# Kernel tuning notes

Hardware: AMD Instinct MI355X
Metric: run time of the kernel (lower is better)

## Reference

```python
import jax, jax.numpy as jnp
import numpy as np

NUM_HEADS = 8
NUM_POINTS = 9


def _bilinear_sample(img, gx, gy):
    """grid_sample, mode=bilinear, padding=zeros, align_corners=True.
    img: (B, C, H, W); gx, gy: (B, M) pixel coords. Returns (B, C, M)."""
    Bc, C, H, W = img.shape
    imgf = img.reshape(Bc, C, H * W)
    x0 = jnp.floor(gx)
    y0 = jnp.floor(gy)
    wx1 = gx - x0
    wy1 = gy - y0

    def corner(xi, yi, w):
        valid = (xi >= 0) & (xi < W) & (yi >= 0) & (yi < H)
        xi_c = jnp.clip(xi, 0, W - 1).astype(jnp.int32)
        yi_c = jnp.clip(yi, 0, H - 1).astype(jnp.int32)
        idx = yi_c * W + xi_c  # (B, M)
        g = jax.vmap(lambda im, ix: im[:, ix])(imgf, idx)  # (B, C, M)
        return g * (w * valid)[:, None, :]

    return (corner(x0, y0, (1 - wx1) * (1 - wy1))
            + corner(x0 + 1, y0, wx1 * (1 - wy1))
            + corner(x0, y0 + 1, (1 - wx1) * wy1)
            + corner(x0 + 1, y0 + 1, wx1 * wy1))


def setup_inputs() -> dict:
    key = jax.random.key(0)
    ks = jax.random.split(key, 6)
    B, Hp, Wp, T, D = 4, 64, 64, 3, 256
    N = Hp * Wp
    Hh, P = NUM_HEADS, NUM_POINTS
    x = jax.random.normal(ks[0], (B, N, T, D), dtype=jnp.float32)
    # offset/attn projections: small random (orig inits them to 0, which is degenerate for testing)
    W_off = jax.random.normal(ks[1], (D, Hh * P * 2), dtype=jnp.float32) * 0.01
    b_off = jnp.zeros((Hh * P * 2,), dtype=jnp.float32)
    W_attn = jax.random.normal(ks[2], (D, Hh * P), dtype=jnp.float32) * 0.01
    b_attn = jnp.zeros((Hh * P,), dtype=jnp.float32)
    W_v = jax.random.normal(ks[3], (D, D), dtype=jnp.float32) * 0.02
    b_v = jnp.zeros((D,), dtype=jnp.float32)
    W_o = jax.random.normal(ks[4], (D, D), dtype=jnp.float32) * 0.02
    b_o = jnp.zeros((D,), dtype=jnp.float32)
    return {"x": x, "W_off": W_off, "b_off": b_off, "W_attn": W_attn,
            "b_attn": b_attn, "W_v": W_v, "b_v": b_v, "W_o": W_o,
            "b_o": b_o, "Hp": Hp, "Wp": Wp}


def reference(x, W_off, b_off, W_attn, b_attn, W_v, b_v, W_o, b_o, Hp, Wp):
    B, N, T, D = x.shape
    Hh, P = NUM_HEADS, NUM_POINTS
    dh = D // Hh

    query = x[:, :, T // 2]  # (B, N, D) middle frame
    offset = (query @ W_off + b_off).reshape(B, N, Hh, P, 2)
    attn = jax.nn.softmax((query @ W_attn + b_attn).reshape(B, N, Hh, P), axis=-1)

    # reference points in [-1, 1], xy order (x = width coord)
    gh, gw = jnp.meshgrid(jnp.arange(Hp, dtype=jnp.float32),
                          jnp.arange(Wp, dtype=jnp.float32), indexing='ij')
    ref = jnp.stack([gw, gh], axis=-1).reshape(N, 2)
    ref = ref / jnp.asarray([Wp - 1, Hp - 1], dtype=jnp.float32) * 2 - 1

    loc = ref[None, :, None, None, :] + offset  # (B, N, H, P, 2) normalized

    value = (x @ W_v + b_v).reshape(B, N, T, Hh, dh)
    # (B, H, T, dh, N) -> (B*H*T, dh, Hp, Wp)
    val = jnp.transpose(value, (0, 3, 2, 4, 1)).reshape(B * Hh * T, dh, Hp, Wp)

    # per-(b,h) grid, shared across frames; fold T into batch of the sampler
    grid = jnp.transpose(loc, (0, 2, 1, 3, 4))  # (B, H, N, P, 2)
    grid = jnp.broadcast_to(grid[:, :, None], (B, Hh, T, N, P, 2))
    grid = grid.reshape(B * Hh * T, N * P, 2)
    gx = (grid[..., 0] + 1) * 0.5 * (Wp - 1)
    gy = (grid[..., 1] + 1) * 0.5 * (Hp - 1)

    sampled = _bilinear_sample(val, gx, gy)  # (B*H*T, dh, N*P)
    sampled = sampled.reshape(B, Hh, T, dh, N, P)

    # weighted sum over points, summed over frames
    out = jnp.einsum('bhtdnp,bnhp->bnhd', sampled, attn).reshape(B, N, D)
    return out @ W_o + b_o
```

## Files before the change

kernel.cpp:

```cpp
#include <hip/hip_runtime.h>
#include <hip/hip_bf16.h>
#include <hip/hip_fp16.h>


#define NH_ 8
#define DH_ 32
#define MM_ 16384

typedef __attribute__((ext_vector_type(8))) short bf16x8;
typedef __attribute__((ext_vector_type(4))) short bf16x4;
typedef __attribute__((ext_vector_type(4))) float f32x4;

static __device__ __forceinline__ unsigned short f2bf(float f) {
  unsigned int u = __float_as_uint(f);
  u = (u + 0x7fff + ((u >> 16) & 1)) >> 16;
  return (unsigned short)u;
}
static __device__ __forceinline__ float bf2f(unsigned short h) {
  return __uint_as_float(((unsigned int)h) << 16);
}

__global__ __launch_bounds__(256) void prep(
    const float* __restrict__ x,
    const float* __restrict__ W_off, const float* __restrict__ W_attn,
    const float* __restrict__ W_v, const float* __restrict__ W_o,
    const float* __restrict__ b_off, const float* __restrict__ b_attn,
    unsigned short* __restrict__ ash, unsigned short* __restrict__ asl,
    unsigned short* __restrict__ xmh, unsigned short* __restrict__ xml,
    unsigned short* __restrict__ wvh, unsigned short* __restrict__ wvl,
    unsigned short* __restrict__ wch, unsigned short* __restrict__ wcl,
    unsigned short* __restrict__ woh, unsigned short* __restrict__ wol,
    float* __restrict__ bcat) {
  const int bid = blockIdx.x, t = threadIdx.x;
  if (bid < 4096) {
    const int gid = bid * 256 + t;
    const int row = gid >> 6, c4 = (gid & 63) * 4;
    const float* xr = x + (size_t)row * 768 + c4;
    float4 a0 = *(const float4*)xr;
    float4 a1 = *(const float4*)(xr + 256);
    float4 a2 = *(const float4*)(xr + 512);
    float s[4] = {a0.x + a1.x + a2.x, a0.y + a1.y + a2.y,
                  a0.z + a1.z + a2.z, a0.w + a1.w + a2.w};
    float m[4] = {a1.x, a1.y, a1.z, a1.w};
    bf16x4 shv, slv, mhv, mlv;
#pragma unroll
    for (int j = 0; j < 4; ++j) {
      unsigned short h = f2bf(s[j]);
      shv[j] = (short)h; slv[j] = (short)f2bf(s[j] - bf2f(h));
      unsigned short h2 = f2bf(m[j]);
      mhv[j] = (short)h2; mlv[j] = (short)f2bf(m[j] - bf2f(h2));
    }
    const size_t o = (size_t)row * 256 + c4;
    *(bf16x4*)(ash + o) = shv;  *(bf16x4*)(asl + o) = slv;
    *(bf16x4*)(xmh + o) = mhv;  *(bf16x4*)(xml + o) = mlv;
  } else {
    const int n = bid - 4096;
    {
      float v = W_v[(size_t)t * 256 + n];
      unsigned short h = f2bf(v);
      wvh[n * 256 + t] = h; wvl[n * 256 + t] = f2bf(v - bf2f(h));
    }
    {
      float v = W_o[(size_t)t * 256 + n];
      unsigned short h = f2bf(v);
      woh[n * 256 + t] = h; wol[n * 256 + t] = f2bf(v - bf2f(h));
    }
    if (n < 216) {
      float v = (n < 144) ? W_off[(size_t)t * 144 + n] : W_attn[(size_t)t * 72 + (n - 144)];
      unsigned short h = f2bf(v);
      wch[n * 256 + t] = h; wcl[n * 256 + t] = f2bf(v - bf2f(h));
    }
    if (n == 0 && t < 216) bcat[t] = (t < 144) ? b_off[t] : b_attn[t - 144];
  }
}

__global__ __launch_bounds__(256, 4) void mgemm01(
    const unsigned short* __restrict__ Ahi, const unsigned short* __restrict__ Alo,
    const unsigned short* __restrict__ Xmh, const unsigned short* __restrict__ Xml,
    const unsigned short* __restrict__ Wvh, const unsigned short* __restrict__ Wvl,
    const unsigned short* __restrict__ Wch, const unsigned short* __restrict__ Wcl,
    const float* __restrict__ b_v, const float* __restrict__ bcat,
    __half* __restrict__ valsum, float* __restrict__ proj) {
  __shared__ unsigned short Ah[64][64], Al[64][64], Bh[64][64], Bl[64][64];
  const int mode1 = blockIdx.y >= 4;
  const int n0 = (blockIdx.y & 3) * 64;
  const int m0 = blockIdx.x * 64;
  const int tid = threadIdx.x, wid = tid >> 6, lane = tid & 63;
  const int am = (wid >> 1) * 32, bn = (wid & 1) * 32;
  const int fr = lane & 15, kg = lane >> 4;
  const unsigned short* Ahs = mode1 ? Xmh : Ahi;
  const unsigned short* Als = mode1 ? Xml : Alo;
  const unsigned short* Bhs = mode1 ? Wch : Wvh;
  const unsigned short* Bls = mode1 ? Wcl : Wvl;

  const int r0s = tid >> 3, c0s = tid & 7;
  const int r1s = r0s + 32;
  const int d0s = r0s * 64 + ((c0s ^ (r0s & 7)) * 8);
  const int d1s = r1s * 64 + ((c0s ^ (r1s & 7)) * 8);

  f32x4 acc[2][2];
#pragma unroll
  for (int i = 0; i < 2; ++i)
#pragma unroll
    for (int j = 0; j < 2; ++j) acc[i][j] = (f32x4)(0.f);

  bf16x8 pah[2], pal[2], pbh[2], pbl[2];

#define LOADT01(k0)                                                          \
  {                                                                          \
    size_t a0 = (size_t)(m0 + r0s) * 256 + (k0) + c0s * 8;                   \
    size_t a1 = (size_t)(m0 + r1s) * 256 + (k0) + c0s * 8;                   \
    pah[0] = *(const bf16x8*)(Ahs + a0); pal[0] = *(const bf16x8*)(Als + a0);\
    pah[1] = *(const bf16x8*)(Ahs + a1); pal[1] = *(const bf16x8*)(Als + a1);\
    int nr0 = n0 + r0s, nr1 = n0 + r1s;                                      \
    size_t b0 = (size_t)nr0 * 256 + (k0) + c0s * 8;                          \
    size_t b1 = (size_t)nr1 * 256 + (k0) + c0s * 8;                          \
    if (!mode1 || nr0 < 216) {                                               \
      pbh[0] = *(const bf16x8*)(Bhs + b0); pbl[0] = *(const bf16x8*)(Bls + b0);\
    } else { pbh[0] = (bf16x8)(short)0; pbl[0] = (bf16x8)(short)0; }         \
    if (!mode1 || nr1 < 216) {                                               \
      pbh[1] = *(const bf16x8*)(Bhs + b1); pbl[1] = *(const bf16x8*)(Bls + b1);\
    } else { pbh[1] = (bf16x8)(short)0; pbl[1] = (bf16x8)(short)0; }         \
  }

#define WRITET()                                                             \
  {                                                                          \
    *(bf16x8*)(&Ah[0][0] + d0s) = pah[0]; *(bf16x8*)(&Al[0][0] + d0s) = pal[0];\
    *(bf16x8*)(&Ah[0][0] + d1s) = pah[1]; *(bf16x8*)(&Al[0][0] + d1s) = pal[1];\
    *(bf16x8*)(&Bh[0][0] + d0s) = pbh[0]; *(bf16x8*)(&Bl[0][0] + d0s) = pbl[0];\
    *(bf16x8*)(&Bh[0][0] + d1s) = pbh[1]; *(bf16x8*)(&Bl[0][0] + d1s) = pbl[1];\
  }

#define COMPUTET()                                                           \
  _Pragma("unroll")                                                          \
  for (int ks = 0; ks < 2; ++ks) {                                           \
    const int kc = ks * 4 + kg;                                              \
    bf16x8 ah[2], al[2], bh[2], bl[2];                                       \
    _Pragma("unroll")                                                        \
    for (int mi = 0; mi < 2; ++mi) {                                         \
      int m = am + mi * 16 + fr;                                             \
      int o = m * 64 + ((kc ^ (m & 7)) * 8);                                 \
      ah[mi] = *(const bf16x8*)(&Ah[0][0] + o);                              \
      al[mi] = *(const bf16x8*)(&Al[0][0] + o);                              \
    }                                                                        \
    _Pragma("unroll")                                                        \
    for (int ni = 0; ni < 2; ++ni) {                                         \
      int nn = bn + ni * 16 + fr;                                            \
      int o = nn * 64 + ((kc ^ (nn & 7)) * 8);                               \
      bh[ni] = *(const bf16x8*)(&Bh[0][0] + o);                              \
      bl[ni] = *(const bf16x8*)(&Bl[0][0] + o);                              \
    }                                                                        \
    _Pragma("unroll")                                                        \
    for (int mi = 0; mi < 2; ++mi)                                           \
      _Pragma("unroll")                                                      \
      for (int ni = 0; ni < 2; ++ni) {                                       \
        acc[mi][ni] = __builtin_amdgcn_mfma_f32_16x16x32_bf16(ah[mi], bh[ni], acc[mi][ni], 0, 0, 0);\
        acc[mi][ni] = __builtin_amdgcn_mfma_f32_16x16x32_bf16(ah[mi], bl[ni], acc[mi][ni], 0, 0, 0);\
        acc[mi][ni] = __builtin_amdgcn_mfma_f32_16x16x32_bf16(al[mi], bh[ni], acc[mi][ni], 0, 0, 0);\
      }                                                                      \
  }

  LOADT01(0);
  WRITET();
  __syncthreads();
#pragma unroll
  for (int t = 0; t < 4; ++t) {
    if (t < 3) LOADT01((t + 1) * 64);
    COMPUTET();
    __syncthreads();
    if (t < 3) { WRITET(); __syncthreads(); }
  }

  const int ro = kg * 4;
#pragma unroll
  for (int mi = 0; mi < 2; ++mi)
#pragma unroll
    for (int ni = 0; ni < 2; ++ni) {
      int col = n0 + bn + ni * 16 + fr;
      if (mode1 && col >= 216) continue;
      int rowb = m0 + am + mi * 16 + ro;
      float bv = mode1 ? bcat[col] : b_v[col] * 3.f;
#pragma unroll
      for (int r = 0; r < 4; ++r) {
        int grow = rowb + r;
        float v = acc[mi][ni][r] + bv;
        if (mode1) {
          proj[(size_t)grow * 216 + col] = v;
        } else {
          int b = grow >> 12, nn2 = grow & 4095;
          int h = col >> 5, d = col & 31;
          valsum[(((size_t)(b * NH_ + h) << 12) + nn2) * DH_ + d] = __float2half_rn(v);
        }
      }
    }
#undef LOADT01
#undef WRITET
#undef COMPUTET
}

__global__ __launch_bounds__(256, 4) void mgemm2(
    const unsigned short* __restrict__ Ahi, const unsigned short* __restrict__ Alo,
    const unsigned short* __restrict__ Bhs, const unsigned short* __restrict__ Bls,
    const float* __restrict__ bias, float* __restrict__ Cout) {
  __shared__ unsigned short Ah[64][64], Al[64][64], Bh[64][64], Bl[64][64];
  const int n0 = blockIdx.y * 64;
  const int m0 = blockIdx.x * 64;
  const int tid = threadIdx.x, wid = tid >> 6, lane = tid & 63;
  const int am = (wid >> 1) * 32, bn = (wid & 1) * 32;
  const int fr = lane & 15, kg = lane >> 4;

  const int r0s = tid >> 3, c0s = tid & 7;
  const int r1s = r0s + 32;
  const int d0s = r0s * 64 + ((c0s ^ (r0s & 7)) * 8);
  const int d1s = r1s * 64 + ((c0s ^ (r1s & 7)) * 8);

  f32x4 acc[2][2];
#pragma unroll
  for (int i = 0; i < 2; ++i)
#pragma unroll
    for (int j = 0; j < 2; ++j) acc[i][j] = (f32x4)(0.f);

  bf16x8 pah[2], pal[2], pbh[2], pbl[2];

#define LOADT2(k0)                                                           \
  {                                                                          \
    size_t a0 = (size_t)(m0 + r0s) * 256 + (k0) + c0s * 8;                   \
    size_t a1 = (size_t)(m0 + r1s) * 256 + (k0) + c0s * 8;                   \
    pah[0] = *(const bf16x8*)(Ahi + a0); pal[0] = *(const bf16x8*)(Alo + a0);\
    pah[1] = *(const bf16x8*)(Ahi + a1); pal[1] = *(const bf16x8*)(Alo + a1);\
    size_t b0 = (size_t)(n0 + r0s) * 256 + (k0) + c0s * 8;                   \
    size_t b1 = (size_t)(n0 + r1s) * 256 + (k0) + c0s * 8;                   \
    pbh[0] = *(const bf16x8*)(Bhs + b0); pbl[0] = *(const bf16x8*)(Bls + b0);\
    pbh[1] = *(const bf16x8*)(Bhs + b1); pbl[1] = *(const bf16x8*)(Bls + b1);\
  }

#define WRITET2()                                                            \
  {                                                                          \
    *(bf16x8*)(&Ah[0][0] + d0s) = pah[0]; *(bf16x8*)(&Al[0][0] + d0s) = pal[0];\
    *(bf16x8*)(&Ah[0][0] + d1s) = pah[1]; *(bf16x8*)(&Al[0][0] + d1s) = pal[1];\
    *(bf16x8*)(&Bh[0][0] + d0s) = pbh[0]; *(bf16x8*)(&Bl[0][0] + d0s) = pbl[0];\
    *(bf16x8*)(&Bh[0][0] + d1s) = pbh[1]; *(bf16x8*)(&Bl[0][0] + d1s) = pbl[1];\
  }

#define COMPUTET2()                                                          \
  _Pragma("unroll")                                                          \
  for (int ks = 0; ks < 2; ++ks) {                                           \
    const int kc = ks * 4 + kg;                                              \
    bf16x8 ah[2], al[2], bh[2], bl[2];                                       \
    _Pragma("unroll")                                                        \
    for (int mi = 0; mi < 2; ++mi) {                                         \
      int m = am + mi * 16 + fr;                                             \
      int o = m * 64 + ((kc ^ (m & 7)) * 8);                                 \
      ah[mi] = *(const bf16x8*)(&Ah[0][0] + o);                              \
      al[mi] = *(const bf16x8*)(&Al[0][0] + o);                              \
    }                                                                        \
    _Pragma("unroll")                                                        \
    for (int ni = 0; ni < 2; ++ni) {                                         \
      int nn = bn + ni * 16 + fr;                                            \
      int o = nn * 64 + ((kc ^ (nn & 7)) * 8);                               \
      bh[ni] = *(const bf16x8*)(&Bh[0][0] + o);                              \
      bl[ni] = *(const bf16x8*)(&Bl[0][0] + o);                              \
    }                                                                        \
    _Pragma("unroll")                                                        \
    for (int mi = 0; mi < 2; ++mi)                                           \
      _Pragma("unroll")                                                      \
      for (int ni = 0; ni < 2; ++ni) {                                       \
        acc[mi][ni] = __builtin_amdgcn_mfma_f32_16x16x32_bf16(ah[mi], bh[ni], acc[mi][ni], 0, 0, 0);\
        acc[mi][ni] = __builtin_amdgcn_mfma_f32_16x16x32_bf16(ah[mi], bl[ni], acc[mi][ni], 0, 0, 0);\
        acc[mi][ni] = __builtin_amdgcn_mfma_f32_16x16x32_bf16(al[mi], bh[ni], acc[mi][ni], 0, 0, 0);\
      }                                                                      \
  }

  LOADT2(0);
  WRITET2();
  __syncthreads();
#pragma unroll
  for (int t = 0; t < 4; ++t) {
    if (t < 3) LOADT2((t + 1) * 64);
    COMPUTET2();
    __syncthreads();
    if (t < 3) { WRITET2(); __syncthreads(); }
  }

  const int ro = kg * 4;
#pragma unroll
  for (int mi = 0; mi < 2; ++mi)
#pragma unroll
    for (int ni = 0; ni < 2; ++ni) {
      int col = n0 + bn + ni * 16 + fr;
      int rowb = m0 + am + mi * 16 + ro;
      float bv = bias[col];
#pragma unroll
      for (int r = 0; r < 4; ++r)
        Cout[(size_t)(rowb + r) * 256 + col] = acc[mi][ni][r] + bv;
    }
#undef LOADT2
#undef WRITET2
#undef COMPUTET2
}

struct IW { int idx; float w; };

__global__ __launch_bounds__(256) void sample4(const __half* __restrict__ valsum,
                                               const float* __restrict__ proj,
                                               unsigned short* __restrict__ ihi,
                                               unsigned short* __restrict__ ilo) {
  const int bid = blockIdx.x;
  const int wv = threadIdx.x >> 6;
  const int lane = threadIdx.x & 63;
  const int row = ((bid & 7) << 11) + ((bid >> 3) << 2) + wv;
  const int b = row >> 12, n = row & 4095;

  __shared__ IW cwi[4][72][4];
  __shared__ float sap[4][76];

  const float* pr = proj + (size_t)row * 216;
  if (lane < 8) {
    const float* pa = pr + 144 + lane * 9;
    float lg[9], mx = -1e30f;
#pragma unroll
    for (int p = 0; p < 9; ++p) { lg[p] = pa[p]; mx = fmaxf(mx, lg[p]); }
    float s = 0.f;
#pragma unroll
    for (int p = 0; p < 9; ++p) { lg[p] = __expf(lg[p] - mx); s += lg[p]; }
    float inv = 1.f / s;
#pragma unroll
    for (int p = 0; p < 9; ++p) sap[wv][lane * 9 + p] = lg[p] * inv;
  }
  __syncthreads();
  for (int e = lane; e < 72; e += 64) {
    float ox = pr[e * 2], oy = pr[e * 2 + 1];
    float gx = (float)(n & 63) + ox * 31.5f;
    float gy = (float)(n >> 6) + oy * 31.5f;
    float fx0 = floorf(gx), fy0 = floorf(gy);
    float wx1 = gx - fx0, wy1 = gy - fy0;
    float wx0 = 1.f - wx1, wy0 = 1.f - wy1;
    int x0 = (int)fx0, y0 = (int)fy0, x1 = x0 + 1, y1 = y0 + 1;
    bool vx0 = (x0 >= 0) & (x0 < 64), vx1 = (x1 >= 0) & (x1 < 64);
    bool vy0 = (y0 >= 0) & (y0 < 64), vy1 = (y1 >= 0) & (y1 < 64);
    int x0c = min(max(x0, 0), 63), x1c = min(max(x1, 0), 63);
    int y0c = min(max(y0, 0), 63), y1c = min(max(y1, 0), 63);
    const float a = sap[wv][e];
    cwi[wv][e][0] = IW{(y0c * 64 + x0c) * DH_, (vx0 & vy0) ? wx0 * wy0 * a : 0.f};
    cwi[wv][e][1] = IW{(y0c * 64 + x1c) * DH_, (vx1 & vy0) ? wx1 * wy0 * a : 0.f};
    cwi[wv][e][2] = IW{(y1c * 64 + x0c) * DH_, (vx0 & vy1) ? wx0 * wy1 * a : 0.f};
    cwi[wv][e][3] = IW{(y1c * 64 + x1c) * DH_, (vx1 & vy1) ? wx1 * wy1 * a : 0.f};
  }
  __syncthreads();

  const int h = lane >> 3, d4 = (lane & 7) * 4;
  const __half* vb = valsum + (((size_t)(b * NH_ + h)) << 12) * DH_ + d4;
  float ax = 0.f, ay = 0.f, az = 0.f, aw = 0.f;
#pragma unroll
  for (int pb = 0; pb < 9; pb += 3) {
    float2 v[24]; float w[12];
#pragma unroll
    for (int q = 0; q < 3; ++q) {
      const int hp = h * 9 + pb + q;
#pragma unroll
      for (int c = 0; c < 4; ++c) {
        IW e = cwi[wv][hp][c];
        const __half2* p = (const __half2*)(vb + e.idx);
        v[(q * 4 + c) * 2 + 0] = __half22float2(p[0]);
        v[(q * 4 + c) * 2 + 1] = __half22float2(p[1]);
        w[q * 4 + c] = e.w;
      }
    }
#pragma unroll
    for (int j = 0; j < 12; ++j) {
      ax += w[j] * v[j * 2].x;     ay += w[j] * v[j * 2].y;
      az += w[j] * v[j * 2 + 1].x; aw += w[j] * v[j * 2 + 1].y;
    }
  }
  float av[4] = {ax, ay, az, aw};
  bf16x4 hv, lv;
#pragma unroll
  for (int j = 0; j < 4; ++j) {
    unsigned short hh = f2bf(av[j]);
    hv[j] = (short)hh;
    lv[j] = (short)f2bf(av[j] - bf2f(hh));
  }
  const size_t o = (size_t)row * 256 + lane * 4;
  *(bf16x4*)(ihi + o) = hv;
  *(bf16x4*)(ilo + o) = lv;
}

extern "C" void kernel_launch(void* const* d_in, const int* in_sizes, int n_in,
                              void* d_out, int out_size, void* d_ws, size_t ws_size,
                              hipStream_t stream) {
  const float* x      = (const float*)d_in[0];
  const float* W_off  = (const float*)d_in[1];
  const float* b_off  = (const float*)d_in[2];
  const float* W_attn = (const float*)d_in[3];
  const float* b_attn = (const float*)d_in[4];
  const float* W_v    = (const float*)d_in[5];
  const float* b_v    = (const float*)d_in[6];
  const float* W_o    = (const float*)d_in[7];
  const float* b_o    = (const float*)d_in[8];
  float* out = (float*)d_out;

  __half* valsum = (__half*)d_ws;
  float* proj    = (float*)(valsum + (size_t)MM_ * 256);
  float* bcat    = proj + (size_t)MM_ * 216;
  unsigned short* ash = (unsigned short*)(bcat + 256);
  unsigned short* asl = ash + (size_t)MM_ * 256;
  unsigned short* xmh = asl + (size_t)MM_ * 256;
  unsigned short* xml = xmh + (size_t)MM_ * 256;
  unsigned short* wvh = xml + (size_t)MM_ * 256;
  unsigned short* wvl = wvh + 65536;
  unsigned short* wch = wvl + 65536;
  unsigned short* wcl = wch + 55296;
  unsigned short* woh = wcl + 55296;
  unsigned short* wol = woh + 65536;
  unsigned short* ihi = ash;
  unsigned short* ilo = asl;

  prep<<<dim3(4352), dim3(256), 0, stream>>>(x, W_off, W_attn, W_v, W_o, b_off, b_attn,
                                             ash, asl, xmh, xml,
                                             wvh, wvl, wch, wcl, woh, wol, bcat);
  mgemm01<<<dim3(256, 8), dim3(256), 0, stream>>>(ash, asl, xmh, xml, wvh, wvl, wch, wcl,
                                                  b_v, bcat, valsum, proj);
  sample4<<<dim3(4096), dim3(256), 0, stream>>>(valsum, proj, ihi, ilo);
  mgemm2<<<dim3(256, 4), dim3(256), 0, stream>>>(ihi, ilo, woh, wol, b_o, out);
}
```

Baseline: 162.2 us.

## Switch split-bf16 GEMMs to fp16 and drop low-part weights for value/output

Replaces the bf16 hi/lo split with an fp16 hi/lo split, which has more mantissa bits. This lets the W_v and W_o weights be stored as a single fp16 without a low part, cutting each MFMA group for those GEMMs from three to two products and removing the Bl loads and shared stores. Only the offset/attention projection keeps a three-term product, and both GEMM grids are flattened to 1D with a remapped block order. The sampler now loads fp16x4 vectors directly. fp16 has less range than bf16, and dropping the weight low parts reduces accuracy.

```diff
diff --git a/kernel.cpp b/kernel.cpp
--- a/kernel.cpp
+++ b/kernel.cpp
@@ -1,23 +1,21 @@
 #include <hip/hip_runtime.h>
 #include <hip/hip_bf16.h>
-#include <hip/hip_fp16.h>
 
 
 #define NH_ 8
 #define DH_ 32
 #define MM_ 16384
 
-typedef __attribute__((ext_vector_type(8))) short bf16x8;
-typedef __attribute__((ext_vector_type(4))) short bf16x4;
+typedef __attribute__((ext_vector_type(8))) _Float16 f16x8;
+typedef __attribute__((ext_vector_type(4))) _Float16 f16x4;
 typedef __attribute__((ext_vector_type(4))) float f32x4;
 
-static __device__ __forceinline__ unsigned short f2bf(float f) {
-  unsigned int u = __float_as_uint(f);
-  u = (u + 0x7fff + ((u >> 16) & 1)) >> 16;
-  return (unsigned short)u;
-}
-static __device__ __forceinline__ float bf2f(unsigned short h) {
-  return __uint_as_float(((unsigned int)h) << 16);
+struct HL { _Float16 h, l; };
+static __device__ __forceinline__ HL fsplit(float f) {
+  HL r;
+  r.h = (_Float16)f;
+  r.l = (_Float16)(f - (float)r.h);
+  return r;
 }
 
 __global__ __launch_bounds__(256) void prep(
@@ -25,11 +23,10 @@
     const float* __restrict__ W_off, const float* __restrict__ W_attn,
     const float* __restrict__ W_v, const float* __restrict__ W_o,
     const float* __restrict__ b_off, const float* __restrict__ b_attn,
-    unsigned short* __restrict__ ash, unsigned short* __restrict__ asl,
-    unsigned short* __restrict__ xmh, unsigned short* __restrict__ xml,
-    unsigned short* __restrict__ wvh, unsigned short* __restrict__ wvl,
-    unsigned short* __restrict__ wch, unsigned short* __restrict__ wcl,
-    unsigned short* __restrict__ woh, unsigned short* __restrict__ wol,
+    _Float16* __restrict__ ash, _Float16* __restrict__ asl,
+    _Float16* __restrict__ xmh, _Float16* __restrict__ xml,
+    _Float16* __restrict__ wv, _Float16* __restrict__ wch,
+    _Float16* __restrict__ wcl, _Float16* __restrict__ wo,
     float* __restrict__ bcat) {
   const int bid = blockIdx.x, t = threadIdx.x;
   if (bid < 4096) {
@@ -42,56 +39,50 @@
     float s[4] = {a0.x + a1.x + a2.x, a0.y + a1.y + a2.y,
                   a0.z + a1.z + a2.z, a0.w + a1.w + a2.w};
     float m[4] = {a1.x, a1.y, a1.z, a1.w};
-    bf16x4 shv, slv, mhv, mlv;
+    f16x4 shv, slv, mhv, mlv;
 #pragma unroll
     for (int j = 0; j < 4; ++j) {
-      unsigned short h = f2bf(s[j]);
-      shv[j] = (short)h; slv[j] = (short)f2bf(s[j] - bf2f(h));
-      unsigned short h2 = f2bf(m[j]);
-      mhv[j] = (short)h2; mlv[j] = (short)f2bf(m[j] - bf2f(h2));
+      HL sj = fsplit(s[j]);
+      shv[j] = sj.h; slv[j] = sj.l;
+      HL mj = fsplit(m[j]);
+      mhv[j] = mj.h; mlv[j] = mj.l;
     }
     const size_t o = (size_t)row * 256 + c4;
-    *(bf16x4*)(ash + o) = shv;  *(bf16x4*)(asl + o) = slv;
-    *(bf16x4*)(xmh + o) = mhv;  *(bf16x4*)(xml + o) = mlv;
+    *(f16x4*)(ash + o) = shv;  *(f16x4*)(asl + o) = slv;
+    *(f16x4*)(xmh + o) = mhv;  *(f16x4*)(xml + o) = mlv;
   } else {
     const int n = bid - 4096;
-    {
-      float v = W_v[(size_t)t * 256 + n];
-      unsigned short h = f2bf(v);
-      wvh[n * 256 + t] = h; wvl[n * 256 + t] = f2bf(v - bf2f(h));
-    }
-    {
-      float v = W_o[(size_t)t * 256 + n];
-      unsigned short h = f2bf(v);
-      woh[n * 256 + t] = h; wol[n * 256 + t] = f2bf(v - bf2f(h));
-    }
+    wv[n * 256 + t] = (_Float16)W_v[(size_t)t * 256 + n];
+    wo[n * 256 + t] = (_Float16)W_o[(size_t)t * 256 + n];
     if (n < 216) {
       float v = (n < 144) ? W_off[(size_t)t * 144 + n] : W_attn[(size_t)t * 72 + (n - 144)];
-      unsigned short h = f2bf(v);
-      wch[n * 256 + t] = h; wcl[n * 256 + t] = f2bf(v - bf2f(h));
+      HL w = fsplit(v);
+      wch[n * 256 + t] = w.h; wcl[n * 256 + t] = w.l;
     }
     if (n == 0 && t < 216) bcat[t] = (t < 144) ? b_off[t] : b_attn[t - 144];
   }
 }
 
 __global__ __launch_bounds__(256, 4) void mgemm01(
-    const unsigned short* __restrict__ Ahi, const unsigned short* __restrict__ Alo,
-    const unsigned short* __restrict__ Xmh, const unsigned short* __restrict__ Xml,
-    const unsigned short* __restrict__ Wvh, const unsigned short* __restrict__ Wvl,
-    const unsigned short* __restrict__ Wch, const unsigned short* __restrict__ Wcl,
+    const _Float16* __restrict__ Ahi, const _Float16* __restrict__ Alo,
+    const _Float16* __restrict__ Xmh, const _Float16* __restrict__ Xml,
+    const _Float16* __restrict__ Wv, const _Float16* __restrict__ Wch,
+    const _Float16* __restrict__ Wcl,
     const float* __restrict__ b_v, const float* __restrict__ bcat,
-    __half* __restrict__ valsum, float* __restrict__ proj) {
-  __shared__ unsigned short Ah[64][64], Al[64][64], Bh[64][64], Bl[64][64];
-  const int mode1 = blockIdx.y >= 4;
-  const int n0 = (blockIdx.y & 3) * 64;
-  const int m0 = blockIdx.x * 64;
+    _Float16* __restrict__ valsum, float* __restrict__ proj) {
+  __shared__ _Float16 Ah[64][64], Al[64][64], Bh[64][64], Bl[64][64];
+  const int bid = blockIdx.x;
+  const int flat = (bid & 7) * 256 + (bid >> 3);
+  const int m0 = (flat >> 3) * 64;
+  const int yy = flat & 7;
+  const int mode1 = yy >= 4;
+  const int n0 = (yy & 3) * 64;
   const int tid = threadIdx.x, wid = tid >> 6, lane = tid & 63;
   const int am = (wid >> 1) * 32, bn = (wid & 1) * 32;
   const int fr = lane & 15, kg = lane >> 4;
-  const unsigned short* Ahs = mode1 ? Xmh : Ahi;
-  const unsigned short* Als = mode1 ? Xml : Alo;
-  const unsigned short* Bhs = mode1 ? Wch : Wvh;
-  const unsigned short* Bls = mode1 ? Wcl : Wvl;
+  const _Float16* Ahs = mode1 ? Xmh : Ahi;
+  const _Float16* Als = mode1 ? Xml : Alo;
+  const _Float16* Bhs = mode1 ? Wch : Wv;
 
   const int r0s = tid >> 3, c0s = tid & 7;
   const int r1s = r0s + 32;
@@ -104,60 +95,66 @@
 #pragma unroll
     for (int j = 0; j < 2; ++j) acc[i][j] = (f32x4)(0.f);
 
-  bf16x8 pah[2], pal[2], pbh[2], pbl[2];
+  f16x8 pah[2], pal[2], pbh[2], pbl[2];
 
 #define LOADT01(k0)                                                          \
   {                                                                          \
     size_t a0 = (size_t)(m0 + r0s) * 256 + (k0) + c0s * 8;                   \
     size_t a1 = (size_t)(m0 + r1s) * 256 + (k0) + c0s * 8;                   \
-    pah[0] = *(const bf16x8*)(Ahs + a0); pal[0] = *(const bf16x8*)(Als + a0);\
-    pah[1] = *(const bf16x8*)(Ahs + a1); pal[1] = *(const bf16x8*)(Als + a1);\
+    pah[0] = *(const f16x8*)(Ahs + a0); pal[0] = *(const f16x8*)(Als + a0);  \
+    pah[1] = *(const f16x8*)(Ahs + a1); pal[1] = *(const f16x8*)(Als + a1);  \
     int nr0 = n0 + r0s, nr1 = n0 + r1s;                                      \
     size_t b0 = (size_t)nr0 * 256 + (k0) + c0s * 8;                          \
     size_t b1 = (size_t)nr1 * 256 + (k0) + c0s * 8;                          \
-    if (!mode1 || nr0 < 216) {                                               \
-      pbh[0] = *(const bf16x8*)(Bhs + b0); pbl[0] = *(const bf16x8*)(Bls + b0);\
-    } else { pbh[0] = (bf16x8)(short)0; pbl[0] = (bf16x8)(short)0; }         \
-    if (!mode1 || nr1 < 216) {                                               \
-      pbh[1] = *(const bf16x8*)(Bhs + b1); pbl[1] = *(const bf16x8*)(Bls + b1);\
-    } else { pbh[1] = (bf16x8)(short)0; pbl[1] = (bf16x8)(short)0; }         \
+    if (!mode1 || nr0 < 216) pbh[0] = *(const f16x8*)(Bhs + b0);             \
+    else pbh[0] = (f16x8)(_Float16)0.f;                                      \
+    if (!mode1 || nr1 < 216) pbh[1] = *(const f16x8*)(Bhs + b1);             \
+    else pbh[1] = (f16x8)(_Float16)0.f;                                      \
+    if (mode1) {                                                             \
+      pbl[0] = (nr0 < 216) ? *(const f16x8*)(Wcl + b0) : (f16x8)(_Float16)0.f;\
+      pbl[1] = (nr1 < 216) ? *(const f16x8*)(Wcl + b1) : (f16x8)(_Float16)0.f;\
+    }                                                                        \
   }
 
 #define WRITET()                                                             \
   {                                                                          \
-    *(bf16x8*)(&Ah[0][0] + d0s) = pah[0]; *(bf16x8*)(&Al[0][0] + d0s) = pal[0];\
-    *(bf16x8*)(&Ah[0][0] + d1s) = pah[1]; *(bf16x8*)(&Al[0][0] + d1s) = pal[1];\
-    *(bf16x8*)(&Bh[0][0] + d0s) = pbh[0]; *(bf16x8*)(&Bl[0][0] + d0s) = pbl[0];\
-    *(bf16x8*)(&Bh[0][0] + d1s) = pbh[1]; *(bf16x8*)(&Bl[0][0] + d1s) = pbl[1];\
+    *(f16x8*)(&Ah[0][0] + d0s) = pah[0]; *(f16x8*)(&Al[0][0] + d0s) = pal[0];\
+    *(f16x8*)(&Ah[0][0] + d1s) = pah[1]; *(f16x8*)(&Al[0][0] + d1s) = pal[1];\
+    *(f16x8*)(&Bh[0][0] + d0s) = pbh[0]; *(f16x8*)(&Bh[0][0] + d1s) = pbh[1];\
+    if (mode1) {                                                             \
+      *(f16x8*)(&Bl[0][0] + d0s) = pbl[0]; *(f16x8*)(&Bl[0][0] + d1s) = pbl[1];\
+    }                                                                        \
   }
 
 #define COMPUTET()                                                           \
   _Pragma("unroll")                                                          \
   for (int ks = 0; ks < 2; ++ks) {                                           \
     const int kc = ks * 4 + kg;                                              \
-    bf16x8 ah[2], al[2], bh[2], bl[2];                                       \
+    f16x8 ah[2], al[2], bh[2];                                               \
     _Pragma("unroll")                                                        \
     for (int mi = 0; mi < 2; ++mi) {                                         \
       int m = am + mi * 16 + fr;                                             \
       int o = m * 64 + ((kc ^ (m & 7)) * 8);                                 \
-      ah[mi] = *(const bf16x8*)(&Ah[0][0] + o);                              \
-      al[mi] = *(const bf16x8*)(&Al[0][0] + o);                              \
+      ah[mi] = *(const f16x8*)(&Ah[0][0] + o);                               \
+      al[mi] = *(const f16x8*)(&Al[0][0] + o);                               \
     }                                                                        \
     _Pragma("unroll")                                                        \
     for (int ni = 0; ni < 2; ++ni) {                                         \
       int nn = bn + ni * 16 + fr;                                            \
       int o = nn * 64 + ((kc ^ (nn & 7)) * 8);                               \
-      bh[ni] = *(const bf16x8*)(&Bh[0][0] + o);                              \
-      bl[ni] = *(const bf16x8*)(&Bl[0][0] + o);                              \
-    }                                                                        \
-    _Pragma("unroll")                                                        \
-    for (int mi = 0; mi < 2; ++mi)                                           \
+      bh[ni] = *(const f16x8*)(&Bh[0][0] + o);                               \
       _Pragma("unroll")                                                      \
-      for (int ni = 0; ni < 2; ++ni) {                                       \
-        acc[mi][ni] = __builtin_amdgcn_mfma_f32_16x16x32_bf16(ah[mi], bh[ni], acc[mi][ni], 0, 0, 0);\
-        acc[mi][ni] = __builtin_amdgcn_mfma_f32_16x16x32_bf16(ah[mi], bl[ni], acc[mi][ni], 0, 0, 0);\
-        acc[mi][ni] = __builtin_amdgcn_mfma_f32_16x16x32_bf16(al[mi], bh[ni], acc[mi][ni], 0, 0, 0);\
+      for (int mi = 0; mi < 2; ++mi) {                                       \
+        acc[mi][ni] = __builtin_amdgcn_mfma_f32_16x16x32_f16(ah[mi], bh[ni], acc[mi][ni], 0, 0, 0);\
+        acc[mi][ni] = __builtin_amdgcn_mfma_f32_16x16x32_f16(al[mi], bh[ni], acc[mi][ni], 0, 0, 0);\
       }                                                                      \
+      if (mode1) {                                                           \
+        f16x8 bl = *(const f16x8*)(&Bl[0][0] + o);                           \
+        _Pragma("unroll")                                                    \
+        for (int mi = 0; mi < 2; ++mi)                                       \
+          acc[mi][ni] = __builtin_amdgcn_mfma_f32_16x16x32_f16(ah[mi], bl, acc[mi][ni], 0, 0, 0);\
+      }                                                                      \
+    }                                                                        \
   }
 
   LOADT01(0);
@@ -189,7 +186,7 @@
         } else {
           int b = grow >> 12, nn2 = grow & 4095;
           int h = col >> 5, d = col & 31;
-          valsum[(((size_t)(b * NH_ + h) << 12) + nn2) * DH_ + d] = __float2half_rn(v);
+          valsum[(((size_t)(b * NH_ + h) << 12) + nn2) * DH_ + d] = (_Float16)v;
         }
       }
     }
@@ -199,12 +196,14 @@
 }
 
 __global__ __launch_bounds__(256, 4) void mgemm2(
-    const unsigned short* __restrict__ Ahi, const unsigned short* __restrict__ Alo,
-    const unsigned short* __restrict__ Bhs, const unsigned short* __restrict__ Bls,
+    const _Float16* __restrict__ Ahi, const _Float16* __restrict__ Alo,
+    const _Float16* __restrict__ Bhs,
     const float* __restrict__ bias, float* __restrict__ Cout) {
-  __shared__ unsigned short Ah[64][64], Al[64][64], Bh[64][64], Bl[64][64];
-  const int n0 = blockIdx.y * 64;
-  const int m0 = blockIdx.x * 64;
+  __shared__ _Float16 Ah[64][64], Al[64][64], Bh[64][64];
+  const int bid = blockIdx.x;
+  const int flat = (bid & 7) * 128 + (bid >> 3);
+  const int m0 = (flat >> 2) * 64;
+  const int n0 = (flat & 3) * 64;
   const int tid = threadIdx.x, wid = tid >> 6, lane = tid & 63;
   const int am = (wid >> 1) * 32, bn = (wid & 1) * 32;
   const int fr = lane & 15, kg = lane >> 4;
@@ -220,54 +219,50 @@
 #pragma unroll
     for (int j = 0; j < 2; ++j) acc[i][j] = (f32x4)(0.f);
 
-  bf16x8 pah[2], pal[2], pbh[2], pbl[2];
+  f16x8 pah[2], pal[2], pbh[2];
 
 #define LOADT2(k0)                                                           \
   {                                                                          \
     size_t a0 = (size_t)(m0 + r0s) * 256 + (k0) + c0s * 8;                   \
     size_t a1 = (size_t)(m0 + r1s) * 256 + (k0) + c0s * 8;                   \
-    pah[0] = *(const bf16x8*)(Ahi + a0); pal[0] = *(const bf16x8*)(Alo + a0);\
-    pah[1] = *(const bf16x8*)(Ahi + a1); pal[1] = *(const bf16x8*)(Alo + a1);\
+    pah[0] = *(const f16x8*)(Ahi + a0); pal[0] = *(const f16x8*)(Alo + a0);  \
+    pah[1] = *(const f16x8*)(Ahi + a1); pal[1] = *(const f16x8*)(Alo + a1);  \
     size_t b0 = (size_t)(n0 + r0s) * 256 + (k0) + c0s * 8;                   \
     size_t b1 = (size_t)(n0 + r1s) * 256 + (k0) + c0s * 8;                   \
-    pbh[0] = *(const bf16x8*)(Bhs + b0); pbl[0] = *(const bf16x8*)(Bls + b0);\
-    pbh[1] = *(const bf16x8*)(Bhs + b1); pbl[1] = *(const bf16x8*)(Bls + b1);\
+    pbh[0] = *(const f16x8*)(Bhs + b0); pbh[1] = *(const f16x8*)(Bhs + b1);  \
   }
 
 #define WRITET2()                                                            \
   {                                                                          \
-    *(bf16x8*)(&Ah[0][0] + d0s) = pah[0]; *(bf16x8*)(&Al[0][0] + d0s) = pal[0];\
-    *(bf16x8*)(&Ah[0][0] + d1s) = pah[1]; *(bf16x8*)(&Al[0][0] + d1s) = pal[1];\
-    *(bf16x8*)(&Bh[0][0] + d0s) = pbh[0]; *(bf16x8*)(&Bl[0][0] + d0s) = pbl[0];\
-    *(bf16x8*)(&Bh[0][0] + d1s) = pbh[1]; *(bf16x8*)(&Bl[0][0] + d1s) = pbl[1];\
+    *(f16x8*)(&Ah[0][0] + d0s) = pah[0]; *(f16x8*)(&Al[0][0] + d0s) = pal[0];\
+    *(f16x8*)(&Ah[0][0] + d1s) = pah[1]; *(f16x8*)(&Al[0][0] + d1s) = pal[1];\
+    *(f16x8*)(&Bh[0][0] + d0s) = pbh[0]; *(f16x8*)(&Bh[0][0] + d1s) = pbh[1];\
   }
 
 #define COMPUTET2()                                                          \
   _Pragma("unroll")                                                          \
   for (int ks = 0; ks < 2; ++ks) {                                           \
     const int kc = ks * 4 + kg;                                              \
-    bf16x8 ah[2], al[2], bh[2], bl[2];                                       \
+    f16x8 ah[2], al[2], bh[2];                                               \
     _Pragma("unroll")                                                        \
     for (int mi = 0; mi < 2; ++mi) {                                         \
       int m = am + mi * 16 + fr;                                             \
       int o = m * 64 + ((kc ^ (m & 7)) * 8);                                 \
-      ah[mi] = *(const bf16x8*)(&Ah[0][0] + o);                              \
-      al[mi] = *(const bf16x8*)(&Al[0][0] + o);                              \
+      ah[mi] = *(const f16x8*)(&Ah[0][0] + o);                               \
+      al[mi] = *(const f16x8*)(&Al[0][0] + o);                               \
     }                                                                        \
     _Pragma("unroll")                                                        \
     for (int ni = 0; ni < 2; ++ni) {                                         \
       int nn = bn + ni * 16 + fr;                                            \
       int o = nn * 64 + ((kc ^ (nn & 7)) * 8);                               \
-      bh[ni] = *(const bf16x8*)(&Bh[0][0] + o);                              \
-      bl[ni] = *(const bf16x8*)(&Bl[0][0] + o);                              \
+      bh[ni] = *(const f16x8*)(&Bh[0][0] + o);                               \
     }                                                                        \
     _Pragma("unroll")                                                        \
     for (int mi = 0; mi < 2; ++mi)                                           \
       _Pragma("unroll")                                                      \
       for (int ni = 0; ni < 2; ++ni) {                                       \
-        acc[mi][ni] = __builtin_amdgcn_mfma_f32_16x16x32_bf16(ah[mi], bh[ni], acc[mi][ni], 0, 0, 0);\
-        acc[mi][ni] = __builtin_amdgcn_mfma_f32_16x16x32_bf16(ah[mi], bl[ni], acc[mi][ni], 0, 0, 0);\
-        acc[mi][ni] = __builtin_amdgcn_mfma_f32_16x16x32_bf16(al[mi], bh[ni], acc[mi][ni], 0, 0, 0);\
+        acc[mi][ni] = __builtin_amdgcn_mfma_f32_16x16x32_f16(ah[mi], bh[ni], acc[mi][ni], 0, 0, 0);\
+        acc[mi][ni] = __builtin_amdgcn_mfma_f32_16x16x32_f16(al[mi], bh[ni], acc[mi][ni], 0, 0, 0);\
       }                                                                      \
   }
 
@@ -301,10 +296,10 @@
 
 struct IW { int idx; float w; };
 
-__global__ __launch_bounds__(256) void sample4(const __half* __restrict__ valsum,
+__global__ __launch_bounds__(256) void sample4(const _Float16* __restrict__ valsum,
                                                const float* __restrict__ proj,
-                                               unsigned short* __restrict__ ihi,
-                                               unsigned short* __restrict__ ilo) {
+                                               _Float16* __restrict__ ihi,
+                                               _Float16* __restrict__ ilo) {
   const int bid = blockIdx.x;
   const int wv = threadIdx.x >> 6;
   const int lane = threadIdx.x & 63;
@@ -349,40 +344,37 @@
   __syncthreads();
 
   const int h = lane >> 3, d4 = (lane & 7) * 4;
-  const __half* vb = valsum + (((size_t)(b * NH_ + h)) << 12) * DH_ + d4;
+  const _Float16* vb = valsum + (((size_t)(b * NH_ + h)) << 12) * DH_ + d4;
   float ax = 0.f, ay = 0.f, az = 0.f, aw = 0.f;
 #pragma unroll
   for (int pb = 0; pb < 9; pb += 3) {
-    float2 v[24]; float w[12];
+    f16x4 v[12]; float w[12];
 #pragma unroll
     for (int q = 0; q < 3; ++q) {
       const int hp = h * 9 + pb + q;
 #pragma unroll
       for (int c = 0; c < 4; ++c) {
         IW e = cwi[wv][hp][c];
-        const __half2* p = (const __half2*)(vb + e.idx);
-        v[(q * 4 + c) * 2 + 0] = __half22float2(p[0]);
-        v[(q * 4 + c) * 2 + 1] = __half22float2(p[1]);
+        v[q * 4 + c] = *(const f16x4*)(vb + e.idx);
         w[q * 4 + c] = e.w;
       }
     }
 #pragma unroll
     for (int j = 0; j < 12; ++j) {
-      ax += w[j] * v[j * 2].x;     ay += w[j] * v[j * 2].y;
-      az += w[j] * v[j * 2 + 1].x; aw += w[j] * v[j * 2 + 1].y;
+      ax += w[j] * (float)v[j][0]; ay += w[j] * (float)v[j][1];
+      az += w[j] * (float)v[j][2]; aw += w[j] * (float)v[j][3];
     }
   }
   float av[4] = {ax, ay, az, aw};
-  bf16x4 hv, lv;
+  f16x4 hv, lv;
 #pragma unroll
   for (int j = 0; j < 4; ++j) {
-    unsigned short hh = f2bf(av[j]);
-    hv[j] = (short)hh;
-    lv[j] = (short)f2bf(av[j] - bf2f(hh));
+    HL r = fsplit(av[j]);
+    hv[j] = r.h; lv[j] = r.l;
   }
   const size_t o = (size_t)row * 256 + lane * 4;
-  *(bf16x4*)(ihi + o) = hv;
-  *(bf16x4*)(ilo + o) = lv;
+  *(f16x4*)(ihi + o) = hv;
+  *(f16x4*)(ilo + o) = lv;
 }
 
 extern "C" void kernel_launch(void* const* d_in, const int* in_sizes, int n_in,
@@ -399,27 +391,25 @@
   const float* b_o    = (const float*)d_in[8];
   float* out = (float*)d_out;
 
-  __half* valsum = (__half*)d_ws;
+  _Float16* valsum = (_Float16*)d_ws;
   float* proj    = (float*)(valsum + (size_t)MM_ * 256);
   float* bcat    = proj + (size_t)MM_ * 216;
-  unsigned short* ash = (unsigned short*)(bcat + 256);
-  unsigned short* asl = ash + (size_t)MM_ * 256;
-  unsigned short* xmh = asl + (size_t)MM_ * 256;
-  unsigned short* xml = xmh + (size_t)MM_ * 256;
-  unsigned short* wvh = xml + (size_t)MM_ * 256;
-  unsigned short* wvl = wvh + 65536;
-  unsigned short* wch = wvl + 65536;
-  unsigned short* wcl = wch + 55296;
-  unsigned short* woh = wcl + 55296;
-  unsigned short* wol = woh + 65536;
-  unsigned short* ihi = ash;
-  unsigned short* ilo = asl;
+  _Float16* ash = (_Float16*)(bcat + 256);
+  _Float16* asl = ash + (size_t)MM_ * 256;
+  _Float16* xmh = asl + (size_t)MM_ * 256;
+  _Float16* xml = xmh + (size_t)MM_ * 256;
+  _Float16* wv  = xml + (size_t)MM_ * 256;
+  _Float16* wch = wv + 65536;
+  _Float16* wcl = wch + 55296;
+  _Float16* wo  = wcl + 55296;
+  _Float16* ihi = ash;
+  _Float16* ilo = asl;
 
   prep<<<dim3(4352), dim3(256), 0, stream>>>(x, W_off, W_attn, W_v, W_o, b_off, b_attn,
                                              ash, asl, xmh, xml,
-                                             wvh, wvl, wch, wcl, woh, wol, bcat);
-  mgemm01<<<dim3(256, 8), dim3(256), 0, stream>>>(ash, asl, xmh, xml, wvh, wvl, wch, wcl,
-                                                  b_v, bcat, valsum, proj);
+                                             wv, wch, wcl, wo, bcat);
+  mgemm01<<<dim3(2048), dim3(256), 0, stream>>>(ash, asl, xmh, xml, wv, wch, wcl,
+                                                b_v, bcat, valsum, proj);
   sample4<<<dim3(4096), dim3(256), 0, stream>>>(valsum, proj, ihi, ilo);
-  mgemm2<<<dim3(256, 4), dim3(256), 0, stream>>>(ihi, ilo, woh, wol, b_o, out);
-}
+  mgemm2<<<dim3(1024), dim3(256), 0, stream>>>(ihi, ilo, wo, b_o, out);
+}
```

Result: no change. 164.5 us (+1.4%).
